# Optimization experiments

Hardware: AMD Instinct MI355X
Metric: run time of the kernel (lower is better)

Reference implementation:

```python
import jax, jax.numpy as jnp
import numpy as np

D = 768   # embedding_len
NL = 4    # nleft attributes
NR = 4    # nright attributes
LL = 256  # total left tokens
LR = 256  # total right tokens
DE = (NL + NR) * D  # entity-matching highway width


def setup_inputs() -> dict:
    key = jax.random.key(0)
    ks = jax.random.split(key, 12)
    f = lambda k, s: (jax.random.normal(k, s, jnp.float32) * 0.02)
    return {
        "left_emb": jax.random.normal(ks[0], (LL, D), jnp.float32),
        "right_emb": jax.random.normal(ks[1], (LR, D), jnp.float32),
        "Wn_tok": f(ks[2], (D, D)), "bn_tok": jnp.zeros((D,), jnp.float32),
        "Wg_tok": f(ks[3], (D, D)), "bg_tok": jnp.full((D,), -2.0, jnp.float32),
        "W_lin_tok": f(ks[4], (D, 1)), "b_lin_tok": jnp.zeros((1,), jnp.float32),
        "attr_emb_left": f(ks[5], (NL, D)),
        "attr_emb_right": f(ks[6], (NR, D)),
        "Wn_ent": f(ks[7], (DE, DE)), "bn_ent": jnp.zeros((DE,), jnp.float32),
        "Wg_ent": f(ks[8], (DE, DE)), "bg_ent": jnp.full((DE,), -2.0, jnp.float32),
        "W_lin_ent": f(ks[9], (DE, 2)), "b_lin_ent": jnp.zeros((2,), jnp.float32),
        "empty_attr_res": f(ks[10], (D,)),
        # per-attribute token counts; left includes an empty attribute
        "left_attrs_len": jnp.array([100, 80, 76, 0], dtype=jnp.int32),
        "right_attrs_len": jnp.array([64, 64, 64, 64], dtype=jnp.int32),
    }


def _highway(x, Wn, bn, Wg, bg):
    h = jax.nn.relu(x @ Wn + bn)
    g = jax.nn.sigmoid(x @ Wg + bg)
    return h * g + (1.0 - g) * x


def _token_matching(left, right, Wn, bn, Wg, bg, W_lin, b_lin):
    # compare_matrix: [L_left, L_right, D]
    cmp = jnp.abs(left[:, None, :] - right[None, :, :])
    hw = _highway(cmp, Wn, bn, Wg, bg)
    scores = hw @ W_lin + b_lin                     # [Ll, Lr, 1]
    # softmax over dim=1 (right tokens); only argmax is used downstream
    idx = jnp.argmax(scores[..., 0], axis=1)        # [Ll]
    return jnp.take_along_axis(cmp, idx[:, None, None], axis=1)[:, 0, :]  # [Ll, D]


def _attribute_matching(tokens, field_emb, cmp_res, lens, empty_attr):
    # ragged per-attribute softmax-weighted segment reduction
    n = field_emb.shape[0]
    L = tokens.shape[0]
    seg = jnp.repeat(jnp.arange(n), lens, total_repeat_length=L)   # [L]
    scores = jnp.einsum('ld,ld->l', tokens, field_emb[seg])        # [L]
    m = jax.ops.segment_max(scores, seg, num_segments=n)
    e = jnp.exp(scores - m[seg])
    z = jax.ops.segment_sum(e, seg, num_segments=n)
    w = e / z[seg]                                                  # softmax within segment
    reps = jax.ops.segment_sum(w[:, None] * cmp_res, seg, num_segments=n)  # [n, D]
    return jnp.where(lens[:, None] > 0, reps, empty_attr[None, :])


def reference(left_emb, right_emb, Wn_tok, bn_tok, Wg_tok, bg_tok,
              W_lin_tok, b_lin_tok, attr_emb_left, attr_emb_right,
              Wn_ent, bn_ent, Wg_ent, bg_ent, W_lin_ent, b_lin_ent,
              empty_attr_res, left_attrs_len, right_attrs_len):
    left_cmp = _token_matching(left_emb, right_emb, Wn_tok, bn_tok, Wg_tok, bg_tok,
                               W_lin_tok, b_lin_tok)
    right_cmp = _token_matching(right_emb, left_emb, Wn_tok, bn_tok, Wg_tok, bg_tok,
                                W_lin_tok, b_lin_tok)
    left_rep = _attribute_matching(left_emb, attr_emb_left, left_cmp,
                                   left_attrs_len, empty_attr_res)
    right_rep = _attribute_matching(right_emb, attr_emb_right, right_cmp,
                                    right_attrs_len, empty_attr_res)
    concat = jnp.concatenate([left_rep, right_rep], axis=0).reshape(1, -1)  # [1, DE]
    hw = _highway(concat, Wn_ent, bn_ent, Wg_ent, bg_ent)
    logits = hw @ W_lin_ent + b_lin_ent                                     # [1, 2]
    return jax.nn.softmax(logits, axis=1).flatten()                         # [2]
```

## Files before the change

### kernel.cpp

```cpp
#include <hip/hip_runtime.h>
#include <math.h>

#define DD 768
#define NT 256
#define DE 6144

typedef _Float16 half8 __attribute__((ext_vector_type(8)));
typedef float floatx4 __attribute__((ext_vector_type(4)));

__global__ __launch_bounds__(256) void transpose_cvt(
    const float* __restrict__ Wn, const float* __restrict__ Wg,
    _Float16* __restrict__ WnT, _Float16* __restrict__ WgT)
{
  const float* W = blockIdx.z ? Wg : Wn;
  _Float16* WT = blockIdx.z ? WgT : WnT;
  __shared__ float tile[32][33];
  const int tx = threadIdx.x & 31, ty = threadIdx.x >> 5;
  const int d0 = blockIdx.x * 32, k0 = blockIdx.y * 32;
  #pragma unroll
  for (int p = 0; p < 4; ++p)
    tile[ty + p*8][tx] = W[(size_t)(k0 + ty + p*8)*DD + d0 + tx];
  __syncthreads();
  #pragma unroll
  for (int p = 0; p < 4; ++p)
    WT[(size_t)(d0 + ty + p*8)*DD + k0 + tx] = (_Float16)tile[tx][ty + p*8];
}

__global__ __launch_bounds__(256, 2) void score_mfma(
    const float* __restrict__ L, const float* __restrict__ R,
    const _Float16* __restrict__ WnT, const _Float16* __restrict__ WgT,
    const float* __restrict__ bn, const float* __restrict__ bg,
    const float* __restrict__ Wl, float* __restrict__ S)
{
  const int jbase = blockIdx.x * 128;
  const int dbase = blockIdx.y * 128;
  const int i     = blockIdx.z;
  const int tid   = threadIdx.x;

  __shared__ _Float16 As [128*72];
  __shared__ _Float16 Bns[128*72];
  __shared__ _Float16 Bgs[128*72];

  floatx4 accn[4][4] = {};
  floatx4 accg[4][4] = {};

  const int kg = tid & 7;
  const int rl = tid >> 3;

  const int lane = tid & 63;
  const int wid  = tid >> 6;
  const int wj = (wid & 1) * 64;
  const int wd = (wid >> 1) * 64;
  const int m = lane & 15;
  const int q = lane >> 4;

  for (int k0 = 0; k0 < DD; k0 += 64) {
    float l0[8];
    *(float4*)&l0[0] = *(const float4*)&L[i*DD + k0 + kg*8];
    *(float4*)&l0[4] = *(const float4*)&L[i*DD + k0 + kg*8 + 4];
    #pragma unroll
    for (int rep = 0; rep < 4; ++rep) {
      const int row = rl + rep*32;
      float rv[8];
      const float* Rrow = &R[(size_t)(jbase + row)*DD + k0 + kg*8];
      *(float4*)&rv[0] = *(const float4*)&Rrow[0];
      *(float4*)&rv[4] = *(const float4*)&Rrow[4];
      half8 h;
      #pragma unroll
      for (int e = 0; e < 8; ++e) h[e] = (_Float16)fabsf(l0[e] - rv[e]);
      *(half8*)&As[row*72 + kg*8] = h;
    }
    #pragma unroll
    for (int rep = 0; rep < 4; ++rep) {
      const int row = rl + rep*32;
      *(half8*)&Bns[row*72 + kg*8] =
          *(const half8*)&WnT[(size_t)(dbase + row)*DD + k0 + kg*8];
      *(half8*)&Bgs[row*72 + kg*8] =
          *(const half8*)&WgT[(size_t)(dbase + row)*DD + k0 + kg*8];
    }
    __syncthreads();
    #pragma unroll
    for (int kk = 0; kk < 64; kk += 32) {
      half8 af[4], bfn[4], bfg[4];
      #pragma unroll
      for (int t4 = 0; t4 < 4; ++t4)
        af[t4] = *(const half8*)&As[(wj + t4*16 + m)*72 + kk + q*8];
      #pragma unroll
      for (int t4 = 0; t4 < 4; ++t4) {
        bfn[t4] = *(const half8*)&Bns[(wd + t4*16 + m)*72 + kk + q*8];
        bfg[t4] = *(const half8*)&Bgs[(wd + t4*16 + m)*72 + kk + q*8];
      }
      #pragma unroll
      for (int tj = 0; tj < 4; ++tj)
        #pragma unroll
        for (int td = 0; td < 4; ++td) {
          accn[tj][td] = __builtin_amdgcn_mfma_f32_16x16x32_f16(
              af[tj], bfn[td], accn[tj][td], 0, 0, 0);
          accg[tj][td] = __builtin_amdgcn_mfma_f32_16x16x32_f16(
              af[tj], bfg[td], accg[tj][td], 0, 0, 0);
        }
    }
    __syncthreads();
  }

  float bnv[4], bgv[4], wlv[4], lv[4];
  int dv[4];
  #pragma unroll
  for (int td = 0; td < 4; ++td) {
    const int d = dbase + wd + td*16 + m;
    dv[td] = d; bnv[td] = bn[d]; bgv[td] = bg[d]; wlv[td] = Wl[d];
    lv[td] = L[i*DD + d];
  }
  const int jb = jbase + wj;
  #pragma unroll
  for (int tj = 0; tj < 4; ++tj) {
    #pragma unroll
    for (int r = 0; r < 4; ++r) {
      const int j = jb + tj*16 + q*4 + r;
      float sc = 0.f;
      #pragma unroll
      for (int td = 0; td < 4; ++td) {
        const float nv = accn[tj][td][r] + bnv[td];
        const float gp = accg[tj][td][r] + bgv[td];
        const float g  = 1.f / (1.f + __expf(-gp));
        const float c  = fabsf(lv[td] - R[(size_t)j*DD + dv[td]]);
        sc += (fmaxf(nv, 0.f)*g + (1.f - g)*c) * wlv[td];
      }
      sc += __shfl_xor(sc, 1, 16);
      sc += __shfl_xor(sc, 2, 16);
      sc += __shfl_xor(sc, 4, 16);
      sc += __shfl_xor(sc, 8, 16);
      if (m == 0) atomicAdd(&S[i*NT + j], sc);
    }
  }
}

__global__ __launch_bounds__(256) void argmax_kernel(const float* __restrict__ S,
    int* __restrict__ idxL, int* __restrict__ idxR)
{
  int b = blockIdx.x;
  int t = threadIdx.x;
  float v = (b < NT) ? S[b*NT + t] : S[t*NT + (b - NT)];
  int idx = t;
  #pragma unroll
  for (int mm = 1; mm < 64; mm <<= 1) {
    float ov = __shfl_xor(v, mm, 64);
    int   oi = __shfl_xor(idx, mm, 64);
    if (ov > v || (ov == v && oi < idx)) { v = ov; idx = oi; }
  }
  __shared__ float sv[4]; __shared__ int si[4];
  if ((t & 63) == 0) { sv[t>>6] = v; si[t>>6] = idx; }
  __syncthreads();
  if (t == 0) {
    #pragma unroll
    for (int w = 1; w < 4; ++w)
      if (sv[w] > v || (sv[w] == v && si[w] < idx)) { v = sv[w]; idx = si[w]; }
    if (b < NT) idxL[b] = idx; else idxR[b - NT] = idx;
  }
}

__global__ __launch_bounds__(256) void attr_score(
    const float* __restrict__ Lemb, const float* __restrict__ Remb,
    const float* __restrict__ AEl, const float* __restrict__ AEr,
    const int* __restrict__ lensL, const int* __restrict__ lensR,
    float* __restrict__ wS, int* __restrict__ segA)
{
  const int side = blockIdx.x;
  const float* tok = side ? Remb : Lemb;
  const float* AE  = side ? AEr  : AEl;
  const int* lens  = side ? lensR : lensL;
  const int t = threadIdx.x;
  const int c0 = lens[0], c1 = c0 + lens[1], c2 = c1 + lens[2];
  const int seg = (t < c0) ? 0 : (t < c1) ? 1 : (t < c2) ? 2 : 3;
  float s = 0.f;
  const float4* tr = (const float4*)&tok[(size_t)t*DD];
  const float4* ar = (const float4*)&AE[(size_t)seg*DD];
  for (int k = 0; k < DD/4; ++k) {
    float4 a = tr[k], b = ar[k];
    s += a.x*b.x + a.y*b.y + a.z*b.z + a.w*b.w;
  }
  __shared__ float scS[NT]; __shared__ int segS[NT];
  __shared__ float mS[4], zS[4];
  scS[t] = s; segS[t] = seg;
  __syncthreads();
  if (t < 4) {
    float m = -INFINITY;
    for (int u = 0; u < NT; ++u) if (segS[u] == t) m = fmaxf(m, scS[u]);
    mS[t] = m;
    float z = 0.f;
    for (int u = 0; u < NT; ++u) if (segS[u] == t) z += __expf(scS[u] - m);
    zS[t] = z;
  }
  __syncthreads();
  wS[side*NT + t] = __expf(s - mS[seg]) / zS[seg];
  segA[side*NT + t] = seg;
}

__global__ __launch_bounds__(256) void attr_reduce(
    const float* __restrict__ Lemb, const float* __restrict__ Remb,
    const int* __restrict__ lensL, const int* __restrict__ lensR,
    const int* __restrict__ idxL, const int* __restrict__ idxR,
    const float* __restrict__ wS, const int* __restrict__ segA,
    const float* __restrict__ empty, float* __restrict__ x)
{
  const int side = blockIdx.x;
  const float* tok = side ? Remb : Lemb;
  const float* oth = side ? Lemb : Remb;
  const int* lens  = side ? lensR : lensL;
  const int* idx   = side ? idxR  : idxL;
  const float* w   = wS + side*NT;
  const int* sg    = segA + side*NT;
  float* xo = x + side*4*DD;
  const int t = threadIdx.x;
  const int dl = t & 63, uq = t >> 6;
  const int d = blockIdx.y*64 + dl;
  float a0 = 0.f, a1 = 0.f, a2 = 0.f, a3 = 0.f;
  for (int u = uq*64; u < uq*64 + 64; ++u) {
    const float c = fabsf(tok[(size_t)u*DD + d] - oth[(size_t)idx[u]*DD + d]);
    const float wc = w[u] * c;
    const int s = sg[u];
    a0 += (s == 0) ? wc : 0.f;
    a1 += (s == 1) ? wc : 0.f;
    a2 += (s == 2) ? wc : 0.f;
    a3 += (s == 3) ? wc : 0.f;
  }
  __shared__ float red[4][4][64];
  red[uq][0][dl] = a0; red[uq][1][dl] = a1;
  red[uq][2][dl] = a2; red[uq][3][dl] = a3;
  __syncthreads();
  if (uq == 0) {
    #pragma unroll
    for (int s = 0; s < 4; ++s) {
      float v = red[0][s][dl] + red[1][s][dl] + red[2][s][dl] + red[3][s][dl];
      xo[s*DD + d] = (lens[s] > 0) ? v : empty[d];
    }
  }
}

__global__ __launch_bounds__(256) void ent_matvec(
    const float* __restrict__ x,
    const float* __restrict__ Wn, const float* __restrict__ Wg,
    float* __restrict__ yn, float* __restrict__ yg)
{
  __shared__ float xs[192];
  const int db = blockIdx.x;
  const int kb = blockIdx.y;
  const int tid = threadIdx.x;
  if (tid < 192) xs[tid] = x[kb*192 + tid];
  __syncthreads();
  const int d = db*256 + tid;
  float an = 0.f, ag = 0.f;
  size_t base = (size_t)kb * 192 * DE + d;
  for (int kk = 0; kk < 192; ++kk) {
    float xv = xs[kk];
    an = fmaf(xv, Wn[base + (size_t)kk*DE], an);
    ag = fmaf(xv, Wg[base + (size_t)kk*DE], ag);
  }
  atomicAdd(&yn[d], an);
  atomicAdd(&yg[d], ag);
}

__global__ __launch_bounds__(256) void final_kernel(
    const float* __restrict__ x, const float* __restrict__ yn,
    const float* __restrict__ yg, const float* __restrict__ bn,
    const float* __restrict__ bg, const float* __restrict__ Wl,
    const float* __restrict__ bl, float* __restrict__ out)
{
  const int tid = threadIdx.x;
  float a0 = 0.f, a1 = 0.f;
  for (int p = 0; p < DE/256; ++p) {
    int d = p*256 + tid;
    float n  = yn[d] + bn[d];
    float gp = yg[d] + bg[d];
    float h  = fmaxf(n, 0.f);
    float g  = 1.f / (1.f + __expf(-gp));
    float hw = h*g + (1.f - g)*x[d];
    a0 += hw * Wl[d*2 + 0];
    a1 += hw * Wl[d*2 + 1];
  }
  #pragma unroll
  for (int mm = 1; mm < 64; mm <<= 1) {
    a0 += __shfl_xor(a0, mm, 64);
    a1 += __shfl_xor(a1, mm, 64);
  }
  __shared__ float s0[4], s1[4];
  if ((tid & 63) == 0) { s0[tid>>6] = a0; s1[tid>>6] = a1; }
  __syncthreads();
  if (tid == 0) {
    for (int w = 1; w < 4; ++w) { a0 += s0[w]; a1 += s1[w]; }
    float l0 = a0 + bl[0], l1 = a1 + bl[1];
    float m = fmaxf(l0, l1);
    float e0 = __expf(l0 - m), e1 = __expf(l1 - m);
    out[0] = e0 / (e0 + e1);
    out[1] = e1 / (e0 + e1);
  }
}

extern "C" void kernel_launch(void* const* d_in, const int* in_sizes, int n_in,
                              void* d_out, int out_size, void* d_ws, size_t ws_size,
                              hipStream_t stream) {
  const float* Lemb   = (const float*)d_in[0];
  const float* Remb   = (const float*)d_in[1];
  const float* Wn_tok = (const float*)d_in[2];
  const float* bn_tok = (const float*)d_in[3];
  const float* Wg_tok = (const float*)d_in[4];
  const float* bg_tok = (const float*)d_in[5];
  const float* Wl_tok = (const float*)d_in[6];
  const float* AEl    = (const float*)d_in[8];
  const float* AEr    = (const float*)d_in[9];
  const float* Wn_ent = (const float*)d_in[10];
  const float* bn_ent = (const float*)d_in[11];
  const float* Wg_ent = (const float*)d_in[12];
  const float* bg_ent = (const float*)d_in[13];
  const float* Wl_ent = (const float*)d_in[14];
  const float* bl_ent = (const float*)d_in[15];
  const float* empty  = (const float*)d_in[16];
  const int*   lensL  = (const int*)d_in[17];
  const int*   lensR  = (const int*)d_in[18];

  char* ws = (char*)d_ws;
  float* S    = (float*)(ws + 0);
  int*  idxL  = (int*)  (ws + 262144);
  int*  idxR  = (int*)  (ws + 263168);
  float* x    = (float*)(ws + 264192);
  float* yn   = (float*)(ws + 288768);
  float* yg   = (float*)(ws + 313344);
  float* wSm  = (float*)(ws + 337920);
  int*  segA  = (int*)  (ws + 339968);
  _Float16* WnT = (_Float16*)(ws + 342016);
  _Float16* WgT = (_Float16*)(ws + 1521664);

  hipMemsetAsync(S, 0, (size_t)NT*NT*sizeof(float), stream);
  hipMemsetAsync(yn, 0, (size_t)2*DE*sizeof(float), stream);

  transpose_cvt<<<dim3(24, 24, 2), 256, 0, stream>>>(Wn_tok, Wg_tok, WnT, WgT);
  score_mfma<<<dim3(2, 6, NT), 256, 0, stream>>>(
      Lemb, Remb, WnT, WgT, bn_tok, bg_tok, Wl_tok, S);
  argmax_kernel<<<512, 256, 0, stream>>>(S, idxL, idxR);
  attr_score<<<2, 256, 0, stream>>>(Lemb, Remb, AEl, AEr, lensL, lensR, wSm, segA);
  attr_reduce<<<dim3(2, 12), 256, 0, stream>>>(
      Lemb, Remb, lensL, lensR, idxL, idxR, wSm, segA, empty, x);
  ent_matvec<<<dim3(24, 32), 256, 0, stream>>>(x, Wn_ent, Wg_ent, yn, yg);
  final_kernel<<<1, 256, 0, stream>>>(
      x, yn, yg, bn_ent, bg_ent, Wl_ent, bl_ent, (float*)d_out);
}
```

Before: 672.8 us.

## Async LDS weight loads with XOR swizzle and vectorized split-K entity matvec

The token-score GEMM now loads the weight tiles straight from global memory into LDS with global_load_lds, and uses an XOR-swizzled layout instead of padding. The layout is pre-applied by the transpose kernel, and occupancy is raised to 3 blocks per SM. The entity highway matvec now uses float4 loads over 64 K-splits writing partial sums, plus a separate reduce kernel in place of atomics and the memset. This aims to cut LDS bank conflicts, register staging and load instruction count, at the cost of extra workspace traffic for the partials and possible register pressure.

```diff
diff --git a/kernel.cpp b/kernel.cpp
--- a/kernel.cpp
+++ b/kernel.cpp
@@ -1,5 +1,6 @@
 #include <hip/hip_runtime.h>
 #include <math.h>
+#include <stdint.h>
 
 #define DD 768
 #define NT 256
@@ -7,6 +8,12 @@
 
 typedef _Float16 half8 __attribute__((ext_vector_type(8)));
 typedef float floatx4 __attribute__((ext_vector_type(4)));
+
+__device__ __forceinline__ void async_ld16(const void* g, void* l) {
+  __builtin_amdgcn_global_load_lds(
+      (const __attribute__((address_space(1))) unsigned int*)g,
+      (__attribute__((address_space(3))) unsigned int*)l, 16, 0, 0);
+}
 
 __global__ __launch_bounds__(256) void transpose_cvt(
     const float* __restrict__ Wn, const float* __restrict__ Wg,
@@ -22,11 +29,15 @@
     tile[ty + p*8][tx] = W[(size_t)(k0 + ty + p*8)*DD + d0 + tx];
   __syncthreads();
   #pragma unroll
-  for (int p = 0; p < 4; ++p)
-    WT[(size_t)(d0 + ty + p*8)*DD + k0 + tx] = (_Float16)tile[tx][ty + p*8];
-}
-
-__global__ __launch_bounds__(256, 2) void score_mfma(
+  for (int p = 0; p < 4; ++p) {
+    const int d = d0 + ty + p*8;
+    const int k = k0 + tx;
+    const int idx = d*DD + (k & ~63) + ((((k >> 3) & 7) ^ (d & 7)) << 3) + (k & 7);
+    WT[idx] = (_Float16)tile[tx][ty + p*8];
+  }
+}
+
+__global__ __launch_bounds__(256, 3) void score_mfma(
     const float* __restrict__ L, const float* __restrict__ R,
     const _Float16* __restrict__ WnT, const _Float16* __restrict__ WgT,
     const float* __restrict__ bn, const float* __restrict__ bg,
@@ -37,9 +48,9 @@
   const int i     = blockIdx.z;
   const int tid   = threadIdx.x;
 
-  __shared__ _Float16 As [128*72];
-  __shared__ _Float16 Bns[128*72];
-  __shared__ _Float16 Bgs[128*72];
+  __shared__ _Float16 As [128*64];
+  __shared__ _Float16 Bns[128*64];
+  __shared__ _Float16 Bgs[128*64];
 
   floatx4 accn[4][4] = {};
   floatx4 accg[4][4] = {};
@@ -53,11 +64,30 @@
   const int wd = (wid >> 1) * 64;
   const int m = lane & 15;
   const int q = lane >> 4;
+  const int gq8 = ((q ^ (m & 7)) << 3);
+
+  const int drow = lane >> 3;
+  const int dseg = lane & 7;
+
+  int aoff[4], boff[4];
+  #pragma unroll
+  for (int t4 = 0; t4 < 4; ++t4) {
+    aoff[t4] = (wj + t4*16 + m) * 64;
+    boff[t4] = (wd + t4*16 + m) * 64;
+  }
 
   for (int k0 = 0; k0 < DD; k0 += 64) {
-    float l0[8];
-    *(float4*)&l0[0] = *(const float4*)&L[i*DD + k0 + kg*8];
-    *(float4*)&l0[4] = *(const float4*)&L[i*DD + k0 + kg*8 + 4];
+    #pragma unroll
+    for (int t = 0; t < 4; ++t) {
+      const int row = wid*32 + t*8 + drow;
+      async_ld16(&WnT[(size_t)(dbase + row)*DD + k0 + dseg*8],
+                 &Bns[(wid*32 + t*8)*64]);
+      async_ld16(&WgT[(size_t)(dbase + row)*DD + k0 + dseg*8],
+                 &Bgs[(wid*32 + t*8)*64]);
+    }
+    float l8[8];
+    *(float4*)&l8[0] = *(const float4*)&L[i*DD + k0 + kg*8];
+    *(float4*)&l8[4] = *(const float4*)&L[i*DD + k0 + kg*8 + 4];
     #pragma unroll
     for (int rep = 0; rep < 4; ++rep) {
       const int row = rl + rep*32;
@@ -67,28 +97,20 @@
       *(float4*)&rv[4] = *(const float4*)&Rrow[4];
       half8 h;
       #pragma unroll
-      for (int e = 0; e < 8; ++e) h[e] = (_Float16)fabsf(l0[e] - rv[e]);
-      *(half8*)&As[row*72 + kg*8] = h;
-    }
-    #pragma unroll
-    for (int rep = 0; rep < 4; ++rep) {
-      const int row = rl + rep*32;
-      *(half8*)&Bns[row*72 + kg*8] =
-          *(const half8*)&WnT[(size_t)(dbase + row)*DD + k0 + kg*8];
-      *(half8*)&Bgs[row*72 + kg*8] =
-          *(const half8*)&WgT[(size_t)(dbase + row)*DD + k0 + kg*8];
+      for (int e = 0; e < 8; ++e) h[e] = (_Float16)fabsf(l8[e] - rv[e]);
+      *(half8*)&As[row*64 + ((kg ^ (row & 7)) << 3)] = h;
     }
     __syncthreads();
     #pragma unroll
     for (int kk = 0; kk < 64; kk += 32) {
+      const int ko = kk ^ gq8;
       half8 af[4], bfn[4], bfg[4];
       #pragma unroll
-      for (int t4 = 0; t4 < 4; ++t4)
-        af[t4] = *(const half8*)&As[(wj + t4*16 + m)*72 + kk + q*8];
+      for (int t4 = 0; t4 < 4; ++t4) af[t4] = *(const half8*)&As[aoff[t4] + ko];
       #pragma unroll
       for (int t4 = 0; t4 < 4; ++t4) {
-        bfn[t4] = *(const half8*)&Bns[(wd + t4*16 + m)*72 + kk + q*8];
-        bfg[t4] = *(const half8*)&Bgs[(wd + t4*16 + m)*72 + kk + q*8];
+        bfn[t4] = *(const half8*)&Bns[boff[t4] + ko];
+        bfg[t4] = *(const half8*)&Bgs[boff[t4] + ko];
       }
       #pragma unroll
       for (int tj = 0; tj < 4; ++tj)
@@ -237,27 +259,45 @@
   }
 }
 
-__global__ __launch_bounds__(256) void ent_matvec(
+__global__ __launch_bounds__(256) void ent_matvec4(
     const float* __restrict__ x,
     const float* __restrict__ Wn, const float* __restrict__ Wg,
-    float* __restrict__ yn, float* __restrict__ yg)
-{
-  __shared__ float xs[192];
+    float* __restrict__ pn, float* __restrict__ pg)
+{
+  __shared__ float xs[96];
   const int db = blockIdx.x;
   const int kb = blockIdx.y;
   const int tid = threadIdx.x;
-  if (tid < 192) xs[tid] = x[kb*192 + tid];
-  __syncthreads();
-  const int d = db*256 + tid;
-  float an = 0.f, ag = 0.f;
-  size_t base = (size_t)kb * 192 * DE + d;
-  for (int kk = 0; kk < 192; ++kk) {
-    float xv = xs[kk];
-    an = fmaf(xv, Wn[base + (size_t)kk*DE], an);
-    ag = fmaf(xv, Wg[base + (size_t)kk*DE], ag);
-  }
-  atomicAdd(&yn[d], an);
-  atomicAdd(&yg[d], ag);
+  if (tid < 96) xs[tid] = x[kb*96 + tid];
+  __syncthreads();
+  const int col = db*1024 + tid*4;
+  float4 an = {0.f,0.f,0.f,0.f}, ag = {0.f,0.f,0.f,0.f};
+  const size_t base = (size_t)kb*96*DE + col;
+  #pragma unroll 8
+  for (int kk = 0; kk < 96; ++kk) {
+    const float xv = xs[kk];
+    float4 wn = *(const float4*)&Wn[base + (size_t)kk*DE];
+    float4 wg = *(const float4*)&Wg[base + (size_t)kk*DE];
+    an.x = fmaf(xv, wn.x, an.x); an.y = fmaf(xv, wn.y, an.y);
+    an.z = fmaf(xv, wn.z, an.z); an.w = fmaf(xv, wn.w, an.w);
+    ag.x = fmaf(xv, wg.x, ag.x); ag.y = fmaf(xv, wg.y, ag.y);
+    ag.z = fmaf(xv, wg.z, ag.z); ag.w = fmaf(xv, wg.w, ag.w);
+  }
+  *(float4*)&pn[(size_t)kb*DE + col] = an;
+  *(float4*)&pg[(size_t)kb*DE + col] = ag;
+}
+
+__global__ __launch_bounds__(256) void ent_reduce(
+    const float* __restrict__ pn, const float* __restrict__ pg,
+    float* __restrict__ yn, float* __restrict__ yg)
+{
+  const int o = blockIdx.x*256 + threadIdx.x;
+  float sn = 0.f, sg = 0.f;
+  for (int kb = 0; kb < 64; ++kb) {
+    sn += pn[(size_t)kb*DE + o];
+    sg += pg[(size_t)kb*DE + o];
+  }
+  yn[o] = sn; yg[o] = sg;
 }
 
 __global__ __launch_bounds__(256) void final_kernel(
@@ -329,9 +369,10 @@
   int*  segA  = (int*)  (ws + 339968);
   _Float16* WnT = (_Float16*)(ws + 342016);
   _Float16* WgT = (_Float16*)(ws + 1521664);
+  float* pn   = (float*)(ws + 2701312);
+  float* pg   = (float*)(ws + 4274176);
 
   hipMemsetAsync(S, 0, (size_t)NT*NT*sizeof(float), stream);
-  hipMemsetAsync(yn, 0, (size_t)2*DE*sizeof(float), stream);
 
   transpose_cvt<<<dim3(24, 24, 2), 256, 0, stream>>>(Wn_tok, Wg_tok, WnT, WgT);
   score_mfma<<<dim3(2, 6, NT), 256, 0, stream>>>(
@@ -340,7 +381,8 @@
   attr_score<<<2, 256, 0, stream>>>(Lemb, Remb, AEl, AEr, lensL, lensR, wSm, segA);
   attr_reduce<<<dim3(2, 12), 256, 0, stream>>>(
       Lemb, Remb, lensL, lensR, idxL, idxR, wSm, segA, empty, x);
-  ent_matvec<<<dim3(24, 32), 256, 0, stream>>>(x, Wn_ent, Wg_ent, yn, yg);
+  ent_matvec4<<<dim3(6, 64), 256, 0, stream>>>(x, Wn_ent, Wg_ent, pn, pg);
+  ent_reduce<<<24, 256, 0, stream>>>(pn, pg, yn, yg);
   final_kernel<<<1, 256, 0, stream>>>(
       x, yn, yg, bn_ent, bg_ent, Wl_ent, bl_ent, (float*)d_out);
 }
```

Result: slower. 1.219 ms (+81.2%).
